# Optimization experiments

Hardware: AMD Instinct MI355X
Metric: run time of the kernel (lower is better)

Reference implementation:

```python
import jax, jax.numpy as jnp
import numpy as np

B, C_IN, N, HC = 32, 128, 8192, 64
HEAD_NAMES = ['hm', 'reg', 'height', 'dim', 'rot', 'iou']
HEAD_OUT = [3, 2, 1, 3, 2, 1]
EPS = 1e-5
INIT_BIAS = -2.19


def setup_inputs() -> dict:
    key = jax.random.key(0)
    ks = jax.random.split(key, 16)
    d = {}
    d['ct_feat'] = jax.random.normal(ks[0], (B, C_IN, N), jnp.float32)
    # shared conv (1x1) + BN1d params
    d['sh_w'] = jax.random.normal(ks[1], (HC, C_IN), jnp.float32) * 0.05
    d['sh_b'] = jnp.zeros((HC,), jnp.float32)
    d['sh_g'] = jnp.ones((HC,), jnp.float32)
    d['sh_beta'] = jnp.zeros((HC,), jnp.float32)
    d['sh_mean'] = jax.random.normal(ks[2], (HC,), jnp.float32) * 0.1
    d['sh_var'] = jax.random.uniform(ks[3], (HC,), jnp.float32) + 0.5
    # first conv layer of each SepHead branch (stacked over 6 heads)
    d['head_w1'] = jax.random.normal(ks[4], (6, HC, HC), jnp.float32) * 0.05
    d['head_b1'] = jnp.zeros((6, HC), jnp.float32)
    d['head_g1'] = jnp.ones((6, HC), jnp.float32)
    d['head_beta1'] = jnp.zeros((6, HC), jnp.float32)
    d['head_mean1'] = jax.random.normal(ks[5], (6, HC), jnp.float32) * 0.1
    d['head_var1'] = jax.random.uniform(ks[6], (6, HC), jnp.float32) + 0.5
    # final conv of each branch (distinct out channels)
    for i, (name, c_out) in enumerate(zip(HEAD_NAMES, HEAD_OUT)):
        d[name + '_w'] = jax.random.normal(ks[7 + i], (c_out, HC), jnp.float32) * 0.05
        if name == 'hm':  # hm final bias is filled with init_bias
            d[name + '_b'] = jnp.full((c_out,), INIT_BIAS, jnp.float32)
        else:
            d[name + '_b'] = jnp.zeros((c_out,), jnp.float32)
    return d


def _bn(x, g, b, m, v):
    # x: [B, C, N]; params: [C]
    return (x - m[:, None]) * jax.lax.rsqrt(v[:, None] + EPS) * g[:, None] + b[:, None]


def reference(ct_feat, sh_w, sh_b, sh_g, sh_beta, sh_mean, sh_var,
              head_w1, head_b1, head_g1, head_beta1, head_mean1, head_var1,
              hm_w, hm_b, reg_w, reg_b, height_w, height_b,
              dim_w, dim_b, rot_w, rot_b, iou_w, iou_b):
    # shared_conv: Conv1d(k=1) + BN1d + ReLU
    y = jnp.einsum('oc,bcn->bon', sh_w, ct_feat) + sh_b[:, None]
    y = jax.nn.relu(_bn(y, sh_g, sh_beta, sh_mean, sh_var))  # [B, HC, N]

    # first layer of all 6 head branches, batched over head axis h
    z = jnp.einsum('hoc,bcn->hbon', head_w1, y) + head_b1[:, None, :, None]
    z = (z - head_mean1[:, None, :, None]) * jax.lax.rsqrt(head_var1[:, None, :, None] + EPS)
    z = z * head_g1[:, None, :, None] + head_beta1[:, None, :, None]
    z = jax.nn.relu(z)  # [6, B, HC, N]

    finals = [(hm_w, hm_b), (reg_w, reg_b), (height_w, height_b),
              (dim_w, dim_b), (rot_w, rot_b), (iou_w, iou_b)]
    outs = [jnp.einsum('oc,bcn->bon', w, z[i]) + b[:, None]
            for i, (w, b) in enumerate(finals)]
    # concat in head order [hm(3), reg(2), height(1), dim(3), rot(2), iou(1)] -> [B, 12, N]
    return jnp.concatenate(outs, axis=1)
```

## Files before the change

kernel.cpp:

```cpp
#include <hip/hip_runtime.h>
#include <hip/hip_bf16.h>
#include <cstdint>

typedef __attribute__((ext_vector_type(8))) short bf16x8;
typedef __attribute__((ext_vector_type(4))) float f32x4;

#define NCOL 8192

#define WS_AW 0
#define WS_A1 8192
#define WS_AF 32768
#define WS_U16_TOTAL 38912
#define WS_OFSH 19456
#define WS_OFH  19520
#define WS_BIAS 19904
#define PREP_TOTAL (WS_U16_TOTAL + 464)

union FragU { uint32_t u[4]; bf16x8 v; uint4 q; };

__device__ __forceinline__ uint16_t f2bf(float f) {
  uint32_t x = __builtin_bit_cast(uint32_t, f);
  x += 0x7fffu + ((x >> 16) & 1u);
  return (uint16_t)(x >> 16);
}
__device__ __forceinline__ uint32_t rne_bits(float f) {
  uint32_t x = __builtin_bit_cast(uint32_t, f);
  return x + 0x7fffu + ((x >> 16) & 1u);
}
__device__ __forceinline__ uint32_t pack_bf16(float lo, float hi) {
  return __builtin_amdgcn_perm(rne_bits(hi), rne_bits(lo), 0x07060302u);
}

__global__ __launch_bounds__(256) void ch_prep(
    const float* __restrict__ shw, const float* __restrict__ shb,
    const float* __restrict__ shg, const float* __restrict__ shbeta,
    const float* __restrict__ shmean, const float* __restrict__ shvar,
    const float* __restrict__ w1, const float* __restrict__ b1,
    const float* __restrict__ g1, const float* __restrict__ beta1,
    const float* __restrict__ mean1, const float* __restrict__ var1,
    const float* __restrict__ hm_w, const float* __restrict__ hm_b,
    const float* __restrict__ reg_w, const float* __restrict__ reg_b,
    const float* __restrict__ height_w, const float* __restrict__ height_b,
    const float* __restrict__ dim_w, const float* __restrict__ dim_b,
    const float* __restrict__ rot_w, const float* __restrict__ rot_b,
    const float* __restrict__ iou_w, const float* __restrict__ iou_b,
    uint16_t* __restrict__ wsq)
{
  const int e = blockIdx.x * 256 + threadIdx.x;
  if (e >= PREP_TOTAL) return;
  const int rowbase[6] = {0, 3, 5, 6, 9, 11};
  const int couts[6]   = {3, 2, 1, 3, 2, 1};
  const float* wfp[6]  = {hm_w, reg_w, height_w, dim_w, rot_w, iou_w};

  if (e < WS_A1) {
    const int i = e & 7, q = (e >> 3) & 3, kc = (e >> 5) & 3, m = e >> 7;
    const int k = kc * 32 + q * 8 + i;
    const float sc = shg[m] * rsqrtf(shvar[m] + 1e-5f);
    wsq[e] = f2bf(shw[m * 128 + k] * sc);
  } else if (e < WS_AF) {
    const int e2 = e - WS_A1;
    const int i = e2 & 7, q = (e2 >> 3) & 3, kc = (e2 >> 5) & 1,
              m = (e2 >> 6) & 63, h = e2 >> 12;
    const int k = kc * 32 + q * 8 + i, row = h * 64 + m;
    const float sc = g1[row] * rsqrtf(var1[row] + 1e-5f);
    wsq[e] = f2bf(w1[row * 64 + k] * sc);
  } else if (e < WS_U16_TOTAL) {
    const int e2 = e - WS_AF;
    const int i = e2 & 7, q = (e2 >> 3) & 3, kc = (e2 >> 5) & 1,
              m = (e2 >> 6) & 15, h = e2 >> 10;
    const int k = kc * 32 + q * 8 + i, rr = m - rowbase[h];
    const float v = (rr >= 0 && rr < couts[h]) ? wfp[h][rr * 64 + k] : 0.f;
    wsq[e] = f2bf(v);
  } else {
    const int t2 = e - WS_U16_TOTAL;
    float* wff = (float*)wsq;
    float v = 0.f;
    if (t2 < 64) {
      const float sc = shg[t2] * rsqrtf(shvar[t2] + 1e-5f);
      v = (shb[t2] - shmean[t2]) * sc + shbeta[t2];
    } else if (t2 < 448) {
      const int i = t2 - 64;
      const float sc = g1[i] * rsqrtf(var1[i] + 1e-5f);
      v = (b1[i] - mean1[i]) * sc + beta1[i];
    } else {
      const int i = t2 - 448;
      if (i < 3)       v = hm_b[i];
      else if (i < 5)  v = reg_b[i - 3];
      else if (i < 6)  v = height_b[i - 5];
      else if (i < 9)  v = dim_b[i - 6];
      else if (i < 11) v = rot_b[i - 9];
      else if (i < 12) v = iou_b[i - 11];
    }
    wff[WS_OFSH + t2] = v;
  }
}

__global__ __launch_bounds__(256, 4) void ch_main(
    const float* __restrict__ ct,
    const uint16_t* __restrict__ wsq,
    const float* __restrict__ wsf,
    float* __restrict__ outp)
{
  __shared__ __align__(16) uint32_t sm_y[4608];
  __shared__ __align__(16) uint32_t sm_z[4608];

  const int t    = threadIdx.x;
  const int wv   = t >> 6;
  const int lane = t & 63;
  const int l15  = lane & 15;
  const int qd   = lane >> 4;
  const int bid  = blockIdx.x;
  const int b    = bid >> 6;
  const int col0 = (bid & 63) * 128;
  const int nb   = wv * 32;

  const float* ctb = ct + (size_t)b * 128 * NCOL;
  const int voff0 = qd * 8 * NCOL + col0 + nb + l15;

  f32x4 accY[4][2];
  #pragma unroll
  for (int mt = 0; mt < 4; ++mt)
    #pragma unroll
    for (int j = 0; j < 2; ++j)
      accY[mt][j] = (f32x4){0.f, 0.f, 0.f, 0.f};

  #pragma unroll
  for (int kc = 0; kc < 4; ++kc) {
    bf16x8 a[4];
    #pragma unroll
    for (int mt = 0; mt < 4; ++mt) {
      FragU fa;
      fa.q = *(const uint4*)(wsq + WS_AW + ((mt * 16 + l15) * 4 + kc) * 32 + qd * 8);
      a[mt] = fa.v;
    }
    #pragma unroll
    for (int j = 0; j < 2; ++j) {
      FragU f;
      #pragma unroll
      for (int i2 = 0; i2 < 4; ++i2) {
        const size_t off = (size_t)((kc * 32 + 2 * i2) * NCOL) + voff0 + j * 16;
        f.u[i2] = pack_bf16(ctb[off], ctb[off + NCOL]);
      }
      #pragma unroll
      for (int mt = 0; mt < 4; ++mt)
        accY[mt][j] = __builtin_amdgcn_mfma_f32_16x16x32_bf16(a[mt], f.v, accY[mt][j], 0, 0, 0);
    }
  }

  #pragma unroll
  for (int mt = 0; mt < 4; ++mt) {
    const f32x4 of = *(const f32x4*)(wsf + WS_OFSH + mt * 16 + qd * 4);
    #pragma unroll
    for (int j = 0; j < 2; ++j) {
      const f32x4 v = accY[mt][j];
      const float y0 = fmaxf(v[0] + of[0], 0.f);
      const float y1 = fmaxf(v[1] + of[1], 0.f);
      const float y2 = fmaxf(v[2] + of[2], 0.f);
      const float y3 = fmaxf(v[3] + of[3], 0.f);
      uint2 val;
      val.x = pack_bf16(y0, y1);
      val.y = pack_bf16(y2, y3);
      *(uint2*)&sm_y[(nb + j * 16 + l15) * 36 + mt * 8 + qd * 2] = val;
    }
  }

  f32x4 accO[2];
  accO[0] = (f32x4){0.f, 0.f, 0.f, 0.f};
  accO[1] = (f32x4){0.f, 0.f, 0.f, 0.f};

  #pragma unroll
  for (int h = 0; h < 6; ++h) {
    f32x4 accZ[4][2];
    #pragma unroll
    for (int mt = 0; mt < 4; ++mt)
      #pragma unroll
      for (int j = 0; j < 2; ++j)
        accZ[mt][j] = (f32x4){0.f, 0.f, 0.f, 0.f};

    #pragma unroll
    for (int kc = 0; kc < 2; ++kc) {
      bf16x8 a[4];
      #pragma unroll
      for (int mt = 0; mt < 4; ++mt) {
        FragU fa;
        fa.q = *(const uint4*)(wsq + WS_A1 + ((h * 64 + mt * 16 + l15) * 2 + kc) * 32 + qd * 8);
        a[mt] = fa.v;
      }
      #pragma unroll
      for (int j = 0; j < 2; ++j) {
        FragU f;
        f.q = *(const uint4*)&sm_y[(nb + j * 16 + l15) * 36 + kc * 16 + qd * 4];
        #pragma unroll
        for (int mt = 0; mt < 4; ++mt)
          accZ[mt][j] = __builtin_amdgcn_mfma_f32_16x16x32_bf16(a[mt], f.v, accZ[mt][j], 0, 0, 0);
      }
    }

    #pragma unroll
    for (int mt = 0; mt < 4; ++mt) {
      const f32x4 of = *(const f32x4*)(wsf + WS_OFH + h * 64 + mt * 16 + qd * 4);
      #pragma unroll
      for (int j = 0; j < 2; ++j) {
        const f32x4 v = accZ[mt][j];
        const float z0 = fmaxf(v[0] + of[0], 0.f);
        const float z1 = fmaxf(v[1] + of[1], 0.f);
        const float z2 = fmaxf(v[2] + of[2], 0.f);
        const float z3 = fmaxf(v[3] + of[3], 0.f);
        uint2 val;
        val.x = pack_bf16(z0, z1);
        val.y = pack_bf16(z2, z3);
        *(uint2*)&sm_z[(nb + j * 16 + l15) * 36 + mt * 8 + qd * 2] = val;
      }
    }

    #pragma unroll
    for (int kc = 0; kc < 2; ++kc) {
      FragU fa;
      fa.q = *(const uint4*)(wsq + WS_AF + ((h * 16 + l15) * 2 + kc) * 32 + qd * 8);
      #pragma unroll
      for (int j = 0; j < 2; ++j) {
        FragU f;
        f.q = *(const uint4*)&sm_z[(nb + j * 16 + l15) * 36 + kc * 16 + qd * 4];
        accO[j] = __builtin_amdgcn_mfma_f32_16x16x32_bf16(fa.v, f.v, accO[j], 0, 0, 0);
      }
    }
  }

  if (qd < 3) {
    const f32x4 bs = *(const f32x4*)(wsf + WS_BIAS + qd * 4);
    #pragma unroll
    for (int j = 0; j < 2; ++j) {
      const int col = col0 + nb + j * 16 + l15;
      #pragma unroll
      for (int r = 0; r < 4; ++r)
        outp[((size_t)(b * 12 + qd * 4 + r)) * NCOL + col] = accO[j][r] + bs[r];
    }
  }
}

extern "C" void kernel_launch(void* const* d_in, const int* in_sizes, int n_in,
                              void* d_out, int out_size, void* d_ws, size_t ws_size,
                              hipStream_t stream) {
  (void)out_size; (void)ws_size;
  static const int sortedPos[25] = {
      0, 24, 19, 21, 20, 22, 23, 8, 3, 5, 4, 6, 7,
      12, 11, 16, 15, 10, 9, 2, 1, 18, 17, 14, 13};
  const bool sorted_order =
      (n_in == 25) && (in_sizes[1] == 3) && (in_sizes[2] == 192) &&
      (in_sizes[8] == 24576) && (in_sizes[24] == 8192);
  const float* p[25];
  for (int r = 0; r < 25; ++r)
    p[r] = (const float*)d_in[sorted_order ? sortedPos[r] : r];

  uint16_t* wsq = (uint16_t*)d_ws;

  hipLaunchKernelGGL(ch_prep, dim3((PREP_TOTAL + 255) / 256), dim3(256), 0, stream,
      p[1], p[2], p[3], p[4], p[5], p[6],
      p[7], p[8], p[9], p[10], p[11], p[12],
      p[13], p[14], p[15], p[16], p[17], p[18],
      p[19], p[20], p[21], p[22], p[23], p[24],
      wsq);

  hipLaunchKernelGGL(ch_main, dim3(2048), dim3(256), 0, stream,
      p[0], (const uint16_t*)wsq, (const float*)wsq, (float*)d_out);
}
```

Measured before the change: 297.7 us.

## Replace LDS staging of intermediate activations with in-register permlane swaps

The shared-conv and per-head hidden activations were previously written to LDS in MFMA-output layout and read back in B-operand layout. Now each wave packs them to bf16 in registers and uses permlane32/permlane16 swaps to rearrange them directly into the fragment layout the next MFMA needs. This drops both LDS buffers and the store/load round trips. Launch bounds are also raised from 4 to 5 waves per SIMD to improve occupancy. The cost is extra cross-lane permute instructions and tighter register pressure.

```diff
diff --git a/kernel.cpp b/kernel.cpp
--- a/kernel.cpp
+++ b/kernel.cpp
@@ -4,6 +4,7 @@
 
 typedef __attribute__((ext_vector_type(8))) short bf16x8;
 typedef __attribute__((ext_vector_type(4))) float f32x4;
+typedef __attribute__((ext_vector_type(2))) int i32x2;
 
 #define NCOL 8192
 
@@ -29,6 +30,14 @@
 }
 __device__ __forceinline__ uint32_t pack_bf16(float lo, float hi) {
   return __builtin_amdgcn_perm(rne_bits(hi), rne_bits(lo), 0x07060302u);
+}
+
+__device__ __forceinline__ void cswap(uint32_t lo, uint32_t hi,
+                                      uint32_t& f1, uint32_t& f2) {
+  i32x2 t = __builtin_amdgcn_permlane32_swap((int)lo, (int)hi, false, false);
+  i32x2 f = __builtin_amdgcn_permlane16_swap(t[0], t[1], false, false);
+  f1 = (uint32_t)f[0];
+  f2 = (uint32_t)f[1];
 }
 
 __global__ __launch_bounds__(256) void ch_prep(
@@ -95,15 +104,12 @@
   }
 }
 
-__global__ __launch_bounds__(256, 4) void ch_main(
+__global__ __launch_bounds__(256, 5) void ch_main(
     const float* __restrict__ ct,
     const uint16_t* __restrict__ wsq,
     const float* __restrict__ wsf,
     float* __restrict__ outp)
 {
-  __shared__ __align__(16) uint32_t sm_y[4608];
-  __shared__ __align__(16) uint32_t sm_z[4608];
-
   const int t    = threadIdx.x;
   const int wv   = t >> 6;
   const int lane = t & 63;
@@ -147,21 +153,23 @@
     }
   }
 
-  #pragma unroll
-  for (int mt = 0; mt < 4; ++mt) {
-    const f32x4 of = *(const f32x4*)(wsf + WS_OFSH + mt * 16 + qd * 4);
-    #pragma unroll
-    for (int j = 0; j < 2; ++j) {
+  FragU yfrag[2][2];
+  #pragma unroll
+  for (int j = 0; j < 2; ++j) {
+    uint32_t P[4][2];
+    #pragma unroll
+    for (int mt = 0; mt < 4; ++mt) {
+      const f32x4 of = *(const f32x4*)(wsf + WS_OFSH + mt * 16 + qd * 4);
       const f32x4 v = accY[mt][j];
-      const float y0 = fmaxf(v[0] + of[0], 0.f);
-      const float y1 = fmaxf(v[1] + of[1], 0.f);
-      const float y2 = fmaxf(v[2] + of[2], 0.f);
-      const float y3 = fmaxf(v[3] + of[3], 0.f);
-      uint2 val;
-      val.x = pack_bf16(y0, y1);
-      val.y = pack_bf16(y2, y3);
-      *(uint2*)&sm_y[(nb + j * 16 + l15) * 36 + mt * 8 + qd * 2] = val;
-    }
+      P[mt][0] = pack_bf16(fmaxf(v[0] + of[0], 0.f), fmaxf(v[1] + of[1], 0.f));
+      P[mt][1] = pack_bf16(fmaxf(v[2] + of[2], 0.f), fmaxf(v[3] + of[3], 0.f));
+    }
+    #pragma unroll
+    for (int kc = 0; kc < 2; ++kc)
+      #pragma unroll
+      for (int u = 0; u < 2; ++u)
+        cswap(P[2 * kc][u], P[2 * kc + 1][u],
+              yfrag[kc][j].u[u], yfrag[kc][j].u[u + 2]);
   }
 
   f32x4 accO[2];
@@ -187,42 +195,37 @@
         a[mt] = fa.v;
       }
       #pragma unroll
-      for (int j = 0; j < 2; ++j) {
-        FragU f;
-        f.q = *(const uint4*)&sm_y[(nb + j * 16 + l15) * 36 + kc * 16 + qd * 4];
+      for (int j = 0; j < 2; ++j)
         #pragma unroll
         for (int mt = 0; mt < 4; ++mt)
-          accZ[mt][j] = __builtin_amdgcn_mfma_f32_16x16x32_bf16(a[mt], f.v, accZ[mt][j], 0, 0, 0);
+          accZ[mt][j] = __builtin_amdgcn_mfma_f32_16x16x32_bf16(a[mt], yfrag[kc][j].v, accZ[mt][j], 0, 0, 0);
+    }
+
+    FragU af[2];
+    #pragma unroll
+    for (int kc = 0; kc < 2; ++kc)
+      af[kc].q = *(const uint4*)(wsq + WS_AF + ((h * 16 + l15) * 2 + kc) * 32 + qd * 8);
+
+    #pragma unroll
+    for (int j = 0; j < 2; ++j) {
+      uint32_t Q[4][2];
+      #pragma unroll
+      for (int mt = 0; mt < 4; ++mt) {
+        const f32x4 of = *(const f32x4*)(wsf + WS_OFH + h * 64 + mt * 16 + qd * 4);
+        const f32x4 v = accZ[mt][j];
+        Q[mt][0] = pack_bf16(fmaxf(v[0] + of[0], 0.f), fmaxf(v[1] + of[1], 0.f));
+        Q[mt][1] = pack_bf16(fmaxf(v[2] + of[2], 0.f), fmaxf(v[3] + of[3], 0.f));
       }
-    }
-
-    #pragma unroll
-    for (int mt = 0; mt < 4; ++mt) {
-      const f32x4 of = *(const f32x4*)(wsf + WS_OFH + h * 64 + mt * 16 + qd * 4);
-      #pragma unroll
-      for (int j = 0; j < 2; ++j) {
-        const f32x4 v = accZ[mt][j];
-        const float z0 = fmaxf(v[0] + of[0], 0.f);
-        const float z1 = fmaxf(v[1] + of[1], 0.f);
-        const float z2 = fmaxf(v[2] + of[2], 0.f);
-        const float z3 = fmaxf(v[3] + of[3], 0.f);
-        uint2 val;
-        val.x = pack_bf16(z0, z1);
-        val.y = pack_bf16(z2, z3);
-        *(uint2*)&sm_z[(nb + j * 16 + l15) * 36 + mt * 8 + qd * 2] = val;
-      }
-    }
-
-    #pragma unroll
-    for (int kc = 0; kc < 2; ++kc) {
-      FragU fa;
-      fa.q = *(const uint4*)(wsq + WS_AF + ((h * 16 + l15) * 2 + kc) * 32 + qd * 8);
-      #pragma unroll
-      for (int j = 0; j < 2; ++j) {
-        FragU f;
-        f.q = *(const uint4*)&sm_z[(nb + j * 16 + l15) * 36 + kc * 16 + qd * 4];
-        accO[j] = __builtin_amdgcn_mfma_f32_16x16x32_bf16(fa.v, f.v, accO[j], 0, 0, 0);
-      }
+      FragU zf[2];
+      #pragma unroll
+      for (int kc = 0; kc < 2; ++kc)
+        #pragma unroll
+        for (int u = 0; u < 2; ++u)
+          cswap(Q[2 * kc][u], Q[2 * kc + 1][u], zf[kc].u[u], zf[kc].u[u + 2]);
+
+      #pragma unroll
+      for (int kc = 0; kc < 2; ++kc)
+        accO[j] = __builtin_amdgcn_mfma_f32_16x16x32_bf16(af[kc].v, zf[kc].v, accO[j], 0, 0, 0);
     }
   }
 
```

Result: slower. 304.9 us (+2.4%).
